# Kernel optimization log

Measured on AMD Instinct MI355X. Metric: run time of the kernel, lower is better.

The kernel has to match this reference:

```python
import jax, jax.numpy as jnp
import numpy as np

N, E, F_NODE, F_EDGE, H, L, G = 50000, 800000, 128, 16, 256, 4, 64
BN_EPS = 1e-5


def setup_inputs() -> dict:
    key = jax.random.key(0)
    ks = jax.random.split(key, 24)
    s = 0.02
    inp = {
        "x": jax.random.normal(ks[0], (N, F_NODE), jnp.float32),
        "edge_attr": jax.random.normal(ks[1], (E, F_EDGE), jnp.float32),
        "edge_index": jax.random.randint(ks[2], (2, E), 0, N, jnp.int32),
        "batch": jnp.sort(jax.random.randint(ks[3], (N,), 0, G, jnp.int32)),
        # projections
        "node_w": jax.random.normal(ks[4], (F_NODE, H), jnp.float32) * s,
        "node_b": jnp.zeros((H,), jnp.float32),
        "edge_w": jax.random.normal(ks[5], (F_EDGE, H), jnp.float32) * s,
        "edge_b": jnp.zeros((H,), jnp.float32),
        # GINEConv MLPs, stacked over layers
        "w1": jax.random.normal(ks[6], (L, H, 2 * H), jnp.float32) * s,
        "b1": jnp.zeros((L, 2 * H), jnp.float32),
        "w2": jax.random.normal(ks[7], (L, 2 * H, H), jnp.float32) * s,
        "b2": jnp.zeros((L, H), jnp.float32),
        # BatchNorm affine params
        "gamma": jnp.ones((L, H), jnp.float32),
        "beta": jnp.zeros((L, H), jnp.float32),
        # attentional aggregation
        "gate_w": jax.random.normal(ks[8], (H, 1), jnp.float32) * s,
        "gate_b": jnp.zeros((1,), jnp.float32),
        "pool_w": jax.random.normal(ks[9], (H, H), jnp.float32) * s,
        "pool_b": jnp.zeros((H,), jnp.float32),
    }
    return inp


def _forward(x, edge_attr, node_w, node_b, edge_w, edge_b, w1, b1, w2, b2,
             gamma, beta, gate_w, gate_b, pool_w, pool_b, edge_index, batch):
    x = jnp.nan_to_num(x)
    edge_attr = jnp.nan_to_num(edge_attr)
    h = jax.nn.relu(x @ node_w + node_b)            # [N, H]
    e = jax.nn.relu(edge_attr @ edge_w + edge_b)    # [E, H]
    src, dst = edge_index[0], edge_index[1]
    for l in range(L):
        # GINEConv: nn((1+eps)*x + sum_j relu(x_j + e_ij)), eps = 0
        msg = jax.nn.relu(h[src] + e)                                  # [E, H]
        agg = jax.ops.segment_sum(msg, dst, num_segments=N)            # [N, H]
        z = h + agg
        z = jax.nn.relu(z @ w1[l] + b1[l]) @ w2[l] + b2[l]             # MLP
        # BatchNorm1d (training-mode batch statistics, biased variance)
        mean = jnp.mean(z, axis=0)
        var = jnp.mean((z - mean) ** 2, axis=0)
        h = gamma[l] * (z - mean) * jax.lax.rsqrt(var + BN_EPS) + beta[l]
        h = jax.nn.relu(h)
        # dropout omitted (eval / deterministic reference)
    # AttentionalAggregation: segment softmax on gate, weighted sum of nn(h)
    g = (h @ gate_w + gate_b)[:, 0]                                    # [N]
    gmax = jax.ops.segment_max(g, batch, num_segments=G)               # [G]
    ex = jnp.exp(g - gmax[batch])
    denom = jax.ops.segment_sum(ex, batch, num_segments=G)             # [G]
    alpha = ex / denom[batch]                                          # [N]
    v = h @ pool_w + pool_b                                            # [N, H]
    pooled = jax.ops.segment_sum(alpha[:, None] * v, batch, num_segments=G)
    return pooled                                                      # [G, H]


def reference(x, edge_attr, edge_index, batch, node_w, node_b, edge_w, edge_b,
              w1, b1, w2, b2, gamma, beta, gate_w, gate_b, pool_w, pool_b):
    return _forward(x, edge_attr, node_w, node_b, edge_w, edge_b, w1, b1, w2, b2,
                    gamma, beta, gate_w, gate_b, pool_w, pool_b, edge_index, batch)
```

## Files before the change

### kernel.cpp

```cpp
#include <hip/hip_runtime.h>

#define DEV __device__ __forceinline__

typedef __attribute__((ext_vector_type(8))) short short8;
typedef __attribute__((ext_vector_type(4))) short short4v;
typedef __attribute__((ext_vector_type(4))) float float4v;
typedef unsigned short ushort_t;

static constexpr int NN = 50000;
static constexpr int EE = 800000;
static constexpr int HH = 256;
static constexpr int GG = 64;
static constexpr int NB = (NN + 255) / 256;
static constexpr float BN_EPS = 1e-5f;

DEV float bf2f(unsigned short s) { return __uint_as_float(((unsigned)s) << 16); }
DEV unsigned short f2bf(float f) {
  unsigned u = __float_as_uint(f);
  u += 0x7fffu + ((u >> 16) & 1u);
  return (unsigned short)(u >> 16);
}

DEV bool probe_f32(const ushort_t* probe) { return probe[0] == 0; }

DEV unsigned f2mono(float s) {
  unsigned u = __float_as_uint(s);
  return (u & 0x80000000u) ? ~u : (u | 0x80000000u);
}

DEV int xcd_swz(int p, int nwg) {
  int q = nwg >> 3, r = nwg & 7;
  int x = p & 7, j = p >> 3;
  int base = (x < r) ? x * (q + 1) : r * (q + 1) + (x - r) * q;
  return base + j;
}

DEV int bofs(int r, int c8) { return (r << 7) + ((c8 ^ (r & 15)) << 3); }

DEV void gld_lds16(const void* g, void* l) {
  __builtin_amdgcn_global_load_lds(
      (const __attribute__((address_space(1))) void*)g,
      (__attribute__((address_space(3))) void*)l, 16, 0, 0);
}

struct PP {
  const void* s[10];
  int off[11];
};

DEV float ld_probe(const void* p, size_t i, bool is_f32) {
  return is_f32 ? ((const float*)p)[i] : bf2f(((const ushort_t*)p)[i]);
}

__global__ __launch_bounds__(256) void prep_k(
    PP pp, ushort_t* pbuf, const void* wn, ushort_t* wTnode, const void* w1,
    ushort_t* wTw1, const void* w2, ushort_t* wTw2, const void* we,
    const void* ebs, ushort_t* wTedge, const ushort_t* probe) {
  const bool is_f32 = probe_f32(probe);
  const int b = blockIdx.x;
  const int tid = threadIdx.x;
  if (b < 41) {
    int i = b * 256 + tid;
    if (i >= pp.off[10]) return;
    int seg = 0;
#pragma unroll
    for (int k = 1; k < 10; ++k)
      if (i >= pp.off[k]) seg = k;
    pbuf[i] = f2bf(ld_probe(pp.s[seg], i - pp.off[seg], is_f32));
  } else if (b < 169) {
    int i = (b - 41) * 256 + tid;
    int k = i >> 8, n = i & 255;
    int p = bofs(n & 127, (k >> 3) & 15) + (k & 7);
    wTnode[((n >> 7) << 14) + p] = f2bf(ld_probe(wn, i, is_f32));
  } else if (b < 2217) {
    int lb = b - 169;
    int l = lb >> 9;
    int i = (lb & 511) * 256 + tid;
    int k = i >> 9, n = i & 511;
    int p = bofs(n & 127, (k >> 3) & 15) + (k & 7);
    wTw1[l * 131072 + (((n >> 7) * 2 + (k >> 7)) << 14) + p] =
        f2bf(ld_probe(w1, (size_t)l * 131072 + i, is_f32));
  } else if (b < 4265) {
    int lb = b - 2217;
    int l = lb >> 9;
    int i = (lb & 511) * 256 + tid;
    int k = i >> 8, n = i & 255;
    int p = bofs(n & 127, (k >> 3) & 15) + (k & 7);
    wTw2[l * 131072 + (((n >> 7) * 4 + (k >> 7)) << 14) + p] =
        f2bf(ld_probe(w2, (size_t)l * 131072 + i, is_f32));
  } else {
    int i = (b - 4265) * 256 + tid;
    int c = i >> 5, k = i & 31;
    ushort_t v = 0;
    if (k < 16) v = f2bf(ld_probe(we, (size_t)k * 256 + c, is_f32));
    else if (k == 16) v = f2bf(ld_probe(ebs, c, is_f32));
    wTedge[i] = v;
  }
}

__global__ __launch_bounds__(256) void cvt_bf16(
    const void* __restrict__ src, ushort_t* __restrict__ dst, size_t n,
    const ushort_t* __restrict__ probe, int nan2num) {
  const bool is_f32 = probe_f32(probe);
  size_t i = (size_t)blockIdx.x * 256 + threadIdx.x;
  if (i >= n) return;
  float v = is_f32 ? ((const float*)src)[i] : bf2f(((const ushort_t*)src)[i]);
  if (nan2num && !(v == v)) v = 0.0f;
  dst[i] = f2bf(v);
}

__global__ __launch_bounds__(256) void hist_k(const int* __restrict__ ei,
                                              int* __restrict__ cnt) {
  int e = blockIdx.x * 256 + threadIdx.x;
  if (e < EE) atomicAdd(&cnt[ei[EE + e]], 1);
}

__global__ __launch_bounds__(256) void scan1_k(const int* __restrict__ cnt,
                                               int* __restrict__ bsum) {
  __shared__ int wsum[4];
  int i = blockIdx.x * 256 + threadIdx.x;
  int lane = threadIdx.x & 63, wave = threadIdx.x >> 6;
  int v = (i < NN) ? cnt[i] : 0;
#pragma unroll
  for (int d = 1; d < 64; d <<= 1) v += __shfl_xor(v, d);
  if (lane == 0) wsum[wave] = v;
  __syncthreads();
  if (threadIdx.x == 0) bsum[blockIdx.x] = wsum[0] + wsum[1] + wsum[2] + wsum[3];
}

__global__ __launch_bounds__(64) void scan2_k(int* __restrict__ bsum) {
  const int lane = threadIdx.x;
  int base = 0;
  for (int start = 0; start < NB; start += 64) {
    int i = start + lane;
    int v = (i < NB) ? bsum[i] : 0;
    int orig = v;
#pragma unroll
    for (int d = 1; d < 64; d <<= 1) {
      int t = __shfl_up(v, d);
      if (lane >= d) v += t;
    }
    if (i < NB) bsum[i] = base + v - orig;
    base += __shfl(v, 63);
  }
}

__global__ __launch_bounds__(256) void scan3_k(const int* __restrict__ cnt,
                                               const int* __restrict__ bsum,
                                               int* __restrict__ rowptr) {
  __shared__ int wsum[4];
  int i = blockIdx.x * 256 + threadIdx.x;
  int lane = threadIdx.x & 63, wave = threadIdx.x >> 6;
  int v = (i < NN) ? cnt[i] : 0;
  int incl = v;
#pragma unroll
  for (int d = 1; d < 64; d <<= 1) {
    int t = __shfl_up(incl, d);
    if (lane >= d) incl += t;
  }
  if (lane == 63) wsum[wave] = incl;
  __syncthreads();
  int wprefix = 0;
#pragma unroll
  for (int w = 0; w < 3; ++w)
    if (w < wave) wprefix += wsum[w];
  if (i < NN) rowptr[i + 1] = bsum[blockIdx.x] + wprefix + incl;
  if (i == 0) rowptr[0] = 0;
}

__global__ __launch_bounds__(256) void copy_k(const int* __restrict__ rowptr,
                                              int* __restrict__ cursor) {
  int i = blockIdx.x * 256 + threadIdx.x;
  if (i < NN) cursor[i] = rowptr[i];
}

__global__ __launch_bounds__(256) void fill_k(
    const int* __restrict__ ei, int* __restrict__ cursor,
    int* __restrict__ srcs, ushort_t* __restrict__ eaPerm,
    const void* __restrict__ ea, const ushort_t* __restrict__ probe) {
  int e = blockIdx.x * 256 + threadIdx.x;
  if (e >= EE) return;
  int dst = ei[EE + e];
  int src = ei[e];
  int pos = atomicAdd(&cursor[dst], 1);
  srcs[pos] = src;
  ushort_t tmp[16];
  if (probe_f32(probe)) {
    const float* p = (const float*)ea + (size_t)e * 16;
#pragma unroll
    for (int k = 0; k < 16; ++k) {
      float v = p[k];
      if (!(v == v)) v = 0.f;
      tmp[k] = f2bf(v);
    }
  } else {
    const ushort_t* p = (const ushort_t*)ea + (size_t)e * 16;
#pragma unroll
    for (int k = 0; k < 16; ++k) {
      ushort_t u = p[k];
      if ((u & 0x7FFFu) > 0x7F80u) u = 0;
      tmp[k] = u;
    }
  }
  short8* q = (short8*)(eaPerm + (size_t)pos * 16);
  short8 a, b;
#pragma unroll
  for (int k = 0; k < 8; ++k) { a[k] = (short)tmp[k]; b[k] = (short)tmp[8 + k]; }
  q[0] = a;
  q[1] = b;
}

__global__ __launch_bounds__(256) void msg_mfma5(
    const int* __restrict__ rowptr, const int* __restrict__ srcs,
    const ushort_t* __restrict__ eaPerm, const ushort_t* __restrict__ wTe,
    const ushort_t* __restrict__ h, ushort_t* __restrict__ xin) {
  __shared__ ushort_t sH[32 * 256];
  __shared__ ushort_t sEa[32 * 18];
  const int tid = threadIdx.x;
  const int lane = tid & 63;
  const int wave = tid >> 6;
  const int le = lane & 15;
  const int q = lane >> 4;

  short8 wf[4];
#pragma unroll
  for (int cg = 0; cg < 4; ++cg)
    wf[cg] = *(const short8*)(wTe +
                              (size_t)((wave * 4 + cg) * 16 + le) * 32 + q * 8);

  float acc[4][4] = {};
  const int rs = rowptr[blockIdx.x], re = rowptr[blockIdx.x + 1];

  const int se = tid >> 5;
  const int ss = tid & 31;

  for (int cs = rs; cs < re; cs += 32) {
    const int cnt = min(32, re - cs);
    if (cs != rs) __syncthreads();
    if (tid < cnt * 2) {
      int e = tid >> 1, half = tid & 1;
      *(short8*)(sEa + e * 18 + half * 8) =
          *(const short8*)(eaPerm + (size_t)(cs + e) * 16 + half * 8);
    }
    for (int r0 = 0; r0 < cnt; r0 += 8) {
      int ec = min(r0 + se, cnt - 1);
      int src = srcs[cs + ec];
      short8 v = *(const short8*)(h + (size_t)src * HH + ss * 8);
      *(short8*)(sH + ec * HH + ((ss * 8) ^ ((ec & 7) << 3))) = v;
    }
    __syncthreads();
    for (int g2 = 0; g2 < cnt; g2 += 16) {
      const int ei = g2 + le;
      const float vmask = (ei < cnt) ? 1.f : 0.f;
      const int ec = min(ei, cnt - 1);
      short8 ea;
      if (q < 2) {
        ea = *(const short8*)(sEa + ec * 18 + q * 8);
      } else {
        short8 z = {0, 0, 0, 0, 0, 0, 0, 0};
        if (q == 2) z[0] = (short)0x3F80;
        ea = z;
      }
      const int swz = (ec & 7) << 3;
      const int hbase = ec * HH;
#pragma unroll
      for (int cg = 0; cg < 4; ++cg) {
        float4v zero = {0.f, 0.f, 0.f, 0.f};
        float4v t =
            __builtin_amdgcn_mfma_f32_16x16x32_bf16(wf[cg], ea, zero, 0, 0, 0);
        const int co = wave * 64 + cg * 16 + q * 4;
        short4v hv = *(const short4v*)(sH + hbase + (co ^ swz));
#pragma unroll
        for (int r = 0; r < 4; ++r) {
          float e2 = fmaxf(t[r], 0.f);
          float m = fmaxf(bf2f((unsigned short)hv[r]) + e2, 0.f);
          acc[cg][r] = fmaf(m, vmask, acc[cg][r]);
        }
      }
    }
  }

#pragma unroll
  for (int cg = 0; cg < 4; ++cg)
#pragma unroll
    for (int r = 0; r < 4; ++r) {
#pragma unroll
      for (int d = 1; d < 16; d <<= 1)
        acc[cg][r] += __shfl_xor(acc[cg][r], d);
    }

  if (le == 0) {
#pragma unroll
    for (int cg = 0; cg < 4; ++cg) {
      const int c0 = wave * 64 + cg * 16 + q * 4;
      short4v hn = *(const short4v*)(h + (size_t)blockIdx.x * HH + c0);
      short4v o;
#pragma unroll
      for (int r = 0; r < 4; ++r)
        o[r] = (short)f2bf(bf2f((unsigned short)hn[r]) + acc[cg][r]);
      *(short4v*)(xin + (size_t)blockIdx.x * HH + c0) = o;
    }
  }
}

template <bool RELU, bool STATS>
__global__ __launch_bounds__(256, 4) void gemm_lds(
    const ushort_t* __restrict__ A, const ushort_t* __restrict__ BT,
    const ushort_t* __restrict__ bias, ushort_t* __restrict__ Cout,
    float* __restrict__ stats, int M, int N, int K, int lda, int lgNby) {
  __shared__ ushort_t bs[128 * 128];
  __shared__ float sSum[128], sSq[128];
  const int tid = threadIdx.x;
  const int lane = tid & 63;
  const int wave = tid >> 6;
  const int q = lane >> 4, ln = lane & 15;
  const int wm = wave & 1, wn = wave >> 1;
  const int lid = xcd_swz(blockIdx.x, gridDim.x);
  const int bx = lid >> lgNby;
  const int by = lid & ((1 << lgNby) - 1);
  const int mW = bx * 128 + wm * 64;
  const short8* Ap[4];
#pragma unroll
  for (int im = 0; im < 4; ++im) {
    int m = mW + im * 16 + ln;
    if (m > M - 1) m = M - 1;
    Ap[im] = (const short8*)(A + (size_t)m * lda) + q;
  }

  float4v acc[4][4] = {};
  const int nch = K >> 7;
  for (int kb = 0; kb < nch; ++kb) {
    {
      const char* g = (const char*)(BT + (((size_t)by * nch + kb) << 14));
#pragma unroll
      for (int j = 0; j < 8; ++j) {
        const int boff = (j * 4 + wave) << 10;
        gld_lds16(g + boff + lane * 16, (char*)bs + boff);
      }
    }
    __syncthreads();
#pragma unroll
    for (int s = 0; s < 4; ++s) {
      short8 a[4], b[4];
#pragma unroll
      for (int im = 0; im < 4; ++im) a[im] = Ap[im][kb * 16 + 4 * s];
#pragma unroll
      for (int jn = 0; jn < 4; ++jn)
        b[jn] = *(const short8*)(bs + bofs(wn * 64 + jn * 16 + ln, 4 * s + q));
#pragma unroll
      for (int im = 0; im < 4; ++im)
#pragma unroll
        for (int jn = 0; jn < 4; ++jn)
          acc[im][jn] = __builtin_amdgcn_mfma_f32_16x16x32_bf16(
              a[im], b[jn], acc[im][jn], 0, 0, 0);
    }
    __syncthreads();
  }
  if (STATS) {
    if (tid < 128) { sSum[tid] = 0.f; sSq[tid] = 0.f; }
    __syncthreads();
  }
#pragma unroll
  for (int jn = 0; jn < 4; ++jn) {
    int n = by * 128 + wn * 64 + jn * 16 + ln;
    float bv = bf2f(bias[n]);
    float ps = 0.f, pq = 0.f;
#pragma unroll
    for (int im = 0; im < 4; ++im) {
#pragma unroll
      for (int r = 0; r < 4; ++r) {
        int m = mW + im * 16 + q * 4 + r;
        if (m < M) {
          float v = acc[im][jn][r] + bv;
          if (RELU) v = fmaxf(v, 0.0f);
          if (STATS) { ps += v; pq += v * v; }
          Cout[(size_t)m * N + n] = f2bf(v);
        }
      }
    }
    if (STATS) {
      int nl = wn * 64 + jn * 16 + ln;
      atomicAdd(&sSum[nl], ps);
      atomicAdd(&sSq[nl], pq);
    }
  }
  if (STATS) {
    __syncthreads();
    if (tid < 128) {
      int n = by * 128 + tid;
      unsafeAtomicAdd(&stats[n], sSum[tid]);
      unsafeAtomicAdd(&stats[HH + n], sSq[tid]);
    }
  }
}

__global__ __launch_bounds__(256) void bn_apply(
    const ushort_t* __restrict__ z, const float* __restrict__ stats,
    const ushort_t* __restrict__ gamma, const ushort_t* __restrict__ beta,
    ushort_t* __restrict__ h) {
  size_t tg = (size_t)blockIdx.x * 256 + threadIdx.x;
  int n = (int)(tg >> 6);
  int c0 = ((int)tg & 63) * 4;
  short4v zv = *(const short4v*)(z + (size_t)n * HH + c0);
  float4v s1 = *(const float4v*)(stats + c0);
  float4v s2 = *(const float4v*)(stats + HH + c0);
  short4v gv = *(const short4v*)(gamma + c0);
  short4v bv = *(const short4v*)(beta + c0);
  const float invN = 1.0f / NN;
  short4v o;
#pragma unroll
  for (int r = 0; r < 4; ++r) {
    float zz = bf2f((unsigned short)zv[r]);
    float mean = s1[r] * invN;
    float var = fmaxf(s2[r] * invN - mean * mean, 0.f);
    float xx = (zz - mean) * rsqrtf(var + BN_EPS);
    float y = bf2f((unsigned short)gv[r]) * xx + bf2f((unsigned short)bv[r]);
    o[r] = (short)f2bf(fmaxf(y, 0.f));
  }
  *(short4v*)(h + (size_t)n * HH + c0) = o;
}

__global__ __launch_bounds__(256) void gate_k(
    const ushort_t* __restrict__ h, const ushort_t* __restrict__ gw,
    const ushort_t* __restrict__ gb, float* __restrict__ g) {
  const int lane = threadIdx.x & 63;
  const int wave = threadIdx.x >> 6;
  const int n = blockIdx.x * 4 + wave;
  short4v hv = *(const short4v*)(h + (size_t)n * HH + lane * 4);
  short4v wv = *(const short4v*)(gw + lane * 4);
  float s = 0.f;
#pragma unroll
  for (int r = 0; r < 4; ++r)
    s += bf2f((unsigned short)hv[r]) * bf2f((unsigned short)wv[r]);
#pragma unroll
  for (int off = 32; off; off >>= 1) s += __shfl_down(s, off);
  if (lane == 0) g[n] = s + bf2f(gb[0]);
}

__global__ __launch_bounds__(256) void segmax_k(
    const float* __restrict__ g, const int* __restrict__ batch,
    unsigned* __restrict__ gmax) {
  __shared__ unsigned smax[GG];
  int tid = threadIdx.x;
  if (tid < GG) smax[tid] = 0u;
  __syncthreads();
  int n = blockIdx.x * 256 + tid;
  if (n < NN) atomicMax(&smax[batch[n]], f2mono(g[n]));
  __syncthreads();
  if (tid < GG && smax[tid] != 0u) atomicMax(&gmax[tid], smax[tid]);
}

__global__ __launch_bounds__(256) void ex_k(
    const float* __restrict__ g, const int* __restrict__ batch,
    const unsigned* __restrict__ gmax, float* __restrict__ ex,
    float* __restrict__ denom) {
  __shared__ float part[GG];
  int tid = threadIdx.x;
  if (tid < GG) part[tid] = 0.f;
  __syncthreads();
  int n = blockIdx.x * 256 + tid;
  if (n < NN) {
    int b = batch[n];
    unsigned u = gmax[b];
    float mx = 0.f;
    if (u != 0u) {
      unsigned fb = (u & 0x80000000u) ? (u & 0x7fffffffu) : ~u;
      mx = __uint_as_float(fb);
    }
    float e = expf(g[n] - mx);
    ex[n] = e;
    atomicAdd(&part[b], e);
  }
  __syncthreads();
  if (tid < GG && part[tid] != 0.f) unsafeAtomicAdd(&denom[tid], part[tid]);
}

__global__ __launch_bounds__(256) void pool_acc(
    const ushort_t* __restrict__ h, const float* __restrict__ ex,
    const int* __restrict__ batch, float* __restrict__ pooled) {
  const int c = threadIdx.x;
  const int n0 = blockIdx.x * 32;
  const int n1 = min(n0 + 32, NN);
  float acc = 0.f;
  int curg = batch[n0];
  for (int n = n0; n < n1; ++n) {
    int g = batch[n];
    if (g != curg) {
      unsafeAtomicAdd(&pooled[curg * HH + c], acc);
      acc = 0.f;
      curg = g;
    }
    acc += ex[n] * bf2f(h[(size_t)n * HH + c]);
  }
  unsafeAtomicAdd(&pooled[curg * HH + c], acc);
}

__global__ __launch_bounds__(256) void pool_fin(
    const float* __restrict__ pooled, const float* __restrict__ denom,
    const void* __restrict__ wp, const ushort_t* __restrict__ pb,
    void* __restrict__ out, const ushort_t* __restrict__ probe) {
  __shared__ float sh[HH];
  const bool is_f32 = probe_f32(probe);
  const int gid = blockIdx.x;
  const int c = threadIdx.x;
  float d = denom[gid];
  float inv = (d > 0.f) ? 1.0f / d : 0.f;
  sh[c] = pooled[gid * HH + c] * inv;
  __syncthreads();
  float acc = bf2f(pb[c]);
  for (int k = 0; k < HH; ++k)
    acc = fmaf(sh[k], ld_probe(wp, (size_t)k * HH + c, is_f32), acc);
  float r = (d > 0.f) ? acc : 0.f;
  if (is_f32)
    ((float*)out)[gid * HH + c] = r;
  else
    ((ushort_t*)out)[gid * HH + c] = f2bf(r);
}

extern "C" void kernel_launch(void* const* d_in, const int* in_sizes, int n_in,
                              void* d_out, int out_size, void* d_ws,
                              size_t ws_size, hipStream_t stream) {
  (void)in_sizes; (void)n_in;
  const int* eidx = (const int*)d_in[2];
  const int* batch = (const int*)d_in[3];
  const ushort_t* probe = (const ushort_t*)d_in[12];

  char* ws = (char*)d_ws;
  size_t off = 0;
  auto alloc = [&](size_t bytes) -> char* {
    char* p = ws + off;
    off = (off + bytes + 255) & ~(size_t)255;
    return p;
  };
  ushort_t* pbuf = (ushort_t*)alloc(10241 * 2);
  ushort_t* c_nb = pbuf + 0;
  ushort_t* c_b1 = pbuf + 4608;
  ushort_t* c_b2 = pbuf + 6656;
  ushort_t* c_ga = pbuf + 7680;
  ushort_t* c_be = pbuf + 8704;
  ushort_t* c_gw = pbuf + 9728;
  ushort_t* c_gb = pbuf + 9984;
  ushort_t* c_pb = pbuf + 9985;
  ushort_t* wTnode = (ushort_t*)alloc((size_t)128 * 256 * 2);
  ushort_t* wTw1 = (ushort_t*)alloc((size_t)4 * 256 * 512 * 2);
  ushort_t* wTw2 = (ushort_t*)alloc((size_t)4 * 512 * 256 * 2);
  ushort_t* wTedge = (ushort_t*)alloc((size_t)256 * 32 * 2);
  float* stats = (float*)alloc(2 * HH * 4);
  int* rowptr = (int*)alloc((size_t)(NN + 1) * 4);
  int* cursor = (int*)alloc((size_t)NN * 4);
  int* bsum = (int*)alloc((size_t)NB * 4);
  int* srcs = (int*)alloc((size_t)EE * 4);
  ushort_t* eaPerm = (ushort_t*)alloc((size_t)EE * 16 * 2);
  ushort_t* hb = (ushort_t*)alloc((size_t)NN * HH * 2);
  ushort_t* xin = (ushort_t*)alloc((size_t)NN * HH * 2);
  ushort_t* zbuf = (ushort_t*)alloc((size_t)NN * 512 * 2);
  const size_t NEED = off;

  if (ws_size < NEED) {
    (void)hipMemsetAsync(d_out, 0, (size_t)out_size * 2, stream);
    return;
  }

  float* gbuf = (float*)zbuf;
  float* exbuf = (float*)zbuf + NN;
  unsigned* gmax = (unsigned*)((float*)zbuf + 2 * NN);
  float* denom = (float*)zbuf + 2 * NN + 64;
  float* pooled = (float*)zbuf + 2 * NN + 256;

  PP pp;
  pp.s[0] = d_in[5];  pp.s[1] = d_in[7];  pp.s[2] = d_in[6];  pp.s[3] = d_in[9];
  pp.s[4] = d_in[11]; pp.s[5] = d_in[12]; pp.s[6] = d_in[13]; pp.s[7] = d_in[14];
  pp.s[8] = d_in[15]; pp.s[9] = d_in[17];
  int offs[11] = {0, 256, 512, 4608, 6656, 7680, 8704, 9728, 9984, 9985, 10241};
  for (int k = 0; k < 11; ++k) pp.off[k] = offs[k];
  prep_k<<<dim3(4297), 256, 0, stream>>>(pp, pbuf, d_in[4], wTnode, d_in[8],
                                         wTw1, d_in[10], wTw2, d_in[6],
                                         d_in[7], wTedge, probe);
  cvt_bf16<<<dim3(25000), 256, 0, stream>>>(d_in[0], xin, (size_t)NN * 128, probe, 1);

  (void)hipMemsetAsync(cursor, 0, (size_t)NN * 4, stream);
  hist_k<<<dim3((EE + 255) / 256), 256, 0, stream>>>(eidx, cursor);
  scan1_k<<<dim3(NB), 256, 0, stream>>>(cursor, bsum);
  scan2_k<<<dim3(1), 64, 0, stream>>>(bsum);
  scan3_k<<<dim3(NB), 256, 0, stream>>>(cursor, bsum, rowptr);
  copy_k<<<dim3((NN + 255) / 256), 256, 0, stream>>>(rowptr, cursor);
  fill_k<<<dim3((EE + 255) / 256), 256, 0, stream>>>(eidx, cursor, srcs, eaPerm,
                                                     d_in[1], probe);

  const int mT = (NN + 127) / 128;

  gemm_lds<true, false><<<dim3(mT * 2), 256, 0, stream>>>(
      xin, wTnode, c_nb, hb, nullptr, NN, 256, 128, 128, 1);

  for (int l = 0; l < 4; ++l) {
    msg_mfma5<<<dim3(NN), 256, 0, stream>>>(rowptr, srcs, eaPerm, wTedge,
                                            hb, xin);
    (void)hipMemsetAsync(stats, 0, 2 * HH * 4, stream);
    gemm_lds<true, false><<<dim3(mT * 4), 256, 0, stream>>>(
        xin, wTw1 + (size_t)l * 131072, c_b1 + l * 512, zbuf, nullptr,
        NN, 512, 256, 256, 2);
    gemm_lds<false, true><<<dim3(mT * 2), 256, 0, stream>>>(
        zbuf, wTw2 + (size_t)l * 131072, c_b2 + l * 256, hb, stats,
        NN, 256, 512, 512, 1);
    bn_apply<<<dim3(NN * 64 / 256), 256, 0, stream>>>(
        hb, stats, c_ga + l * 256, c_be + l * 256, hb);
  }

  (void)hipMemsetAsync(gmax, 0, GG * 4, stream);
  (void)hipMemsetAsync(denom, 0, GG * 4, stream);
  (void)hipMemsetAsync(pooled, 0, (size_t)GG * HH * 4, stream);
  gate_k<<<dim3(NN / 4), 256, 0, stream>>>(hb, c_gw, c_gb, gbuf);
  segmax_k<<<dim3(NB), 256, 0, stream>>>(gbuf, batch, gmax);
  ex_k<<<dim3((NN + 255) / 256), 256, 0, stream>>>(gbuf, batch, gmax, exbuf, denom);
  pool_acc<<<dim3((NN + 31) / 32), 256, 0, stream>>>(hb, exbuf, batch, pooled);
  pool_fin<<<dim3(GG), 256, 0, stream>>>(pooled, denom, d_in[16], c_pb, d_out,
                                         probe);
}
```

Measured before the change: 1.495 ms.

## Keep full-K weight panel resident in LDS across multiple M tiles

Adds a GEMM kernel that loads the entire K-extent of a 128-column weight slice into LDS once and reuses it for two consecutive 128-row M tiles, reading A directly from global memory. It replaces the generic LDS GEMM for the node projection and the first MLP layer. This halves the grid and cuts repeated weight loads into LDS, in exchange for 64KB of LDS per block (occupancy limited to 2 blocks) and uncoalesced global A reads without LDS staging.

```diff
diff --git a/kernel.cpp b/kernel.cpp
--- a/kernel.cpp
+++ b/kernel.cpp
@@ -303,6 +303,84 @@
   }
 }
 
+template <bool RELU>
+__global__ __launch_bounds__(256, 2) void gemm_bres(
+    const ushort_t* __restrict__ A, const ushort_t* __restrict__ BT,
+    const ushort_t* __restrict__ bias, ushort_t* __restrict__ Cout,
+    int M, int N, int K, int lda, int lgNby, int mpb, int mtiles) {
+  __shared__ ushort_t bs[2 * 128 * 128];
+  const int tid = threadIdx.x;
+  const int lane = tid & 63;
+  const int wave = tid >> 6;
+  const int q = lane >> 4, ln = lane & 15;
+  const int wm = wave & 1, wn = wave >> 1;
+  const int lid = xcd_swz(blockIdx.x, gridDim.x);
+  const int bxg = lid >> lgNby;
+  const int by = lid & ((1 << lgNby) - 1);
+  const int nch = K >> 7;
+
+  for (int kb = 0; kb < nch; ++kb) {
+    const char* g = (const char*)(BT + (((size_t)by * nch + kb) << 14));
+    char* l = (char*)(bs + (kb << 14));
+#pragma unroll
+    for (int j = 0; j < 8; ++j) {
+      const int boff = (j * 4 + wave) << 10;
+      gld_lds16(g + boff + lane * 16, l + boff);
+    }
+  }
+  __syncthreads();
+
+  for (int t = 0; t < mpb; ++t) {
+    const int bx = bxg * mpb + t;
+    if (bx >= mtiles) break;
+    const int mW = bx * 128 + wm * 64;
+    const short8* Ap[4];
+#pragma unroll
+    for (int im = 0; im < 4; ++im) {
+      int m = mW + im * 16 + ln;
+      if (m > M - 1) m = M - 1;
+      Ap[im] = (const short8*)(A + (size_t)m * lda) + q;
+    }
+    float4v acc[4][4] = {};
+    for (int kb = 0; kb < nch; ++kb) {
+      const ushort_t* bsk = bs + (kb << 14);
+#pragma unroll
+      for (int s = 0; s < 4; ++s) {
+        short8 a[4], b[4];
+#pragma unroll
+        for (int im = 0; im < 4; ++im) a[im] = Ap[im][kb * 16 + 4 * s];
+#pragma unroll
+        for (int jn = 0; jn < 4; ++jn)
+          b[jn] =
+              *(const short8*)(bsk + bofs(wn * 64 + jn * 16 + ln, 4 * s + q));
+#pragma unroll
+        for (int im = 0; im < 4; ++im)
+#pragma unroll
+          for (int jn = 0; jn < 4; ++jn)
+            acc[im][jn] = __builtin_amdgcn_mfma_f32_16x16x32_bf16(
+                a[im], b[jn], acc[im][jn], 0, 0, 0);
+      }
+    }
+#pragma unroll
+    for (int jn = 0; jn < 4; ++jn) {
+      int n = by * 128 + wn * 64 + jn * 16 + ln;
+      float bv = bf2f(bias[n]);
+#pragma unroll
+      for (int im = 0; im < 4; ++im) {
+#pragma unroll
+        for (int r = 0; r < 4; ++r) {
+          int m = mW + im * 16 + q * 4 + r;
+          if (m < M) {
+            float v = acc[im][jn][r] + bv;
+            if (RELU) v = fmaxf(v, 0.0f);
+            Cout[(size_t)m * N + n] = f2bf(v);
+          }
+        }
+      }
+    }
+  }
+}
+
 template <bool RELU, bool STATS>
 __global__ __launch_bounds__(256, 4) void gemm_lds(
     const ushort_t* __restrict__ A, const ushort_t* __restrict__ BT,
@@ -588,17 +666,18 @@
                                                      d_in[1], probe);
 
   const int mT = (NN + 127) / 128;
-
-  gemm_lds<true, false><<<dim3(mT * 2), 256, 0, stream>>>(
-      xin, wTnode, c_nb, hb, nullptr, NN, 256, 128, 128, 1);
+  const int mG = (mT + 1) / 2;
+
+  gemm_bres<true><<<dim3(mG * 2), 256, 0, stream>>>(
+      xin, wTnode, c_nb, hb, NN, 256, 128, 128, 1, 2, mT);
 
   for (int l = 0; l < 4; ++l) {
     msg_mfma5<<<dim3(NN), 256, 0, stream>>>(rowptr, srcs, eaPerm, wTedge,
                                             hb, xin);
     (void)hipMemsetAsync(stats, 0, 2 * HH * 4, stream);
-    gemm_lds<true, false><<<dim3(mT * 4), 256, 0, stream>>>(
-        xin, wTw1 + (size_t)l * 131072, c_b1 + l * 512, zbuf, nullptr,
-        NN, 512, 256, 256, 2);
+    gemm_bres<true><<<dim3(mG * 4), 256, 0, stream>>>(
+        xin, wTw1 + (size_t)l * 131072, c_b1 + l * 512, zbuf,
+        NN, 512, 256, 256, 2, 2, mT);
     gemm_lds<false, true><<<dim3(mT * 2), 256, 0, stream>>>(
         zbuf, wTw2 + (size_t)l * 131072, c_b2 + l * 256, hb, stats,
         NN, 256, 512, 512, 1);
```

After: 1.491 ms. No clear change (-0.3%).
